# Performance work log

Measured on AMD Instinct MI355X. Metric: run time of the kernel, lower is better.

The kernel has to match this reference:

```python
import jax, jax.numpy as jnp
import numpy as np

D_MODEL = 4096
D_FF = 16384
BATCH = 1
SEQ = 1024


def setup_inputs() -> dict:
    key = jax.random.key(0)
    k_x, k_k, k_s = jax.random.split(key, 3)
    inputs = jax.random.normal(k_x, (BATCH, SEQ, D_MODEL), dtype=jnp.float32)
    # int4 quantized kernel, values in [-8, 8)
    kernel = jax.random.randint(k_k, (D_MODEL, D_FF), -8, 8, dtype=jnp.int32).astype(jnp.int4)
    # per-output-channel scale, shape (1, D_FF), strictly positive
    scale = jax.random.uniform(k_s, (1, D_FF), dtype=jnp.float32, minval=0.5, maxval=2.0)
    return {"inputs": inputs, "kernel": kernel, "scale": scale}


def reference(inputs, kernel, scale):
    # Dequantize: int4 kernel -> fp32, divide by per-channel scale
    kernel_f = kernel.astype(jnp.float32) / scale  # [D_MODEL, D_FF]
    # btd,df->btf
    return jnp.einsum("btd,df->btf", inputs, kernel_f)
```

## Files before the change

### kernel.cpp

```cpp
#include <hip/hip_runtime.h>
#include <hip/hip_bf16.h>

#define D_MODEL 4096
#define D_FF    16384
#define SEQ     1024

typedef __attribute__((ext_vector_type(4))) float          f32x4;
typedef __attribute__((ext_vector_type(4))) float          fvec4;
typedef __attribute__((ext_vector_type(8))) short          bf16x8;
typedef __attribute__((ext_vector_type(4))) unsigned short u16x4;

constexpr int BM = 256, BN = 256, BK = 64;
constexpr int NTHREADS = 512;
constexpr int NT = D_MODEL / BK;

__device__ __forceinline__ unsigned short f2bf(float f) {
    unsigned int u = __builtin_bit_cast(unsigned int, f);
    u += 0x7FFFu + ((u >> 16) & 1u);
    return (unsigned short)(u >> 16);
}

__device__ __forceinline__ float decode_kq(unsigned int w) {
    int iv = (int)w;
    return ((unsigned int)(iv + 8) <= 15u) ? (float)iv
                                           : __builtin_bit_cast(float, w);
}

__global__ __launch_bounds__(NTHREADS, 2)
void int4_gemm_kernel(const float* __restrict__ X, const unsigned int* __restrict__ Kq,
                      const float* __restrict__ scale, float* __restrict__ out)
{
    __shared__ short A_lds[2][BM * BK];
    __shared__ short B_lds[2][BN * BK];

    const int bid = blockIdx.x;
    const int bm  = (bid >> 3) & 3;
    const int bn  = (bid & 7) * 8 + (bid >> 5);

    const int tid  = threadIdx.x;
    const int lane = tid & 63;
    const int w    = tid >> 6;
    const int wr   = w >> 2;
    const int wc   = w & 3;
    const int lrow = lane & 15;
    const int lgrp = lane >> 4;

    const int row0 = bm * BM;
    const int col0 = bn * BN;

    const int a_m  = tid >> 4;
    const int a_f4 = tid & 15;
    const int b_n  = tid & 255;
    const int b_k8 = tid >> 8;

    f32x4 acc[8][4];
    #pragma unroll
    for (int i = 0; i < 8; ++i)
        #pragma unroll
        for (int j = 0; j < 4; ++j)
            acc[i][j] = (f32x4){0.f, 0.f, 0.f, 0.f};

    fvec4        aReg[8];
    unsigned int bReg[4][8];

    auto issue_loads = [&](int kt) {
        const int kbase = kt * BK;
        #pragma unroll
        for (int i = 0; i < 8; ++i) {
            int m = a_m + i * 32;
            aReg[i] = *reinterpret_cast<const fvec4*>(
                &X[(size_t)(row0 + m) * D_MODEL + kbase + a_f4 * 4]);
        }
        #pragma unroll
        for (int i = 0; i < 4; ++i) {
            int k8 = b_k8 + i * 2;
            const unsigned int* src =
                &Kq[(size_t)(kbase + k8 * 8) * D_FF + col0 + b_n];
            #pragma unroll
            for (int j = 0; j < 8; ++j) bReg[i][j] = src[(size_t)j * D_FF];
        }
    };

    auto write_lds = [&](int buf) {
        char* aB = (char*)A_lds[buf];
        char* bB = (char*)B_lds[buf];
        #pragma unroll
        for (int i = 0; i < 8; ++i) {
            int m = a_m + i * 32;
            u16x4 h;
            #pragma unroll
            for (int e = 0; e < 4; ++e) h[e] = f2bf(aReg[i][e]);
            int slot16 = a_f4 >> 1;
            int boff = m * 128 + ((slot16 ^ (m & 7)) * 16) + (a_f4 & 1) * 8;
            *reinterpret_cast<u16x4*>(aB + boff) = h;
        }
        #pragma unroll
        for (int i = 0; i < 4; ++i) {
            int k8 = b_k8 + i * 2;
            bf16x8 h;
            #pragma unroll
            for (int j = 0; j < 8; ++j) h[j] = (short)f2bf(decode_kq(bReg[i][j]));
            int boff = b_n * 128 + ((k8 ^ (b_n & 7)) * 16);
            *reinterpret_cast<bf16x8*>(bB + boff) = h;
        }
    };

    issue_loads(0);

    int cur = 0;
    for (int kt = 0; kt < NT; ++kt) {
        write_lds(cur);
        if (kt + 1 < NT) issue_loads(kt + 1);
        __syncthreads();

        const char* aB = (const char*)A_lds[cur];
        const char* bB = (const char*)B_lds[cur];
        #pragma unroll
        for (int ks = 0; ks < 2; ++ks) {
            bf16x8 afrag[8];
            bf16x8 bfrag[4];
            #pragma unroll
            for (int i = 0; i < 8; ++i) {
                int r = wr * 128 + i * 16 + lrow;
                int s = (ks * 4 + lgrp) ^ (r & 7);
                afrag[i] = *reinterpret_cast<const bf16x8*>(aB + r * 128 + s * 16);
            }
            #pragma unroll
            for (int j = 0; j < 4; ++j) {
                int n = wc * 64 + j * 16 + lrow;
                int s = (ks * 4 + lgrp) ^ (n & 7);
                bfrag[j] = *reinterpret_cast<const bf16x8*>(bB + n * 128 + s * 16);
            }
            #pragma unroll
            for (int i = 0; i < 8; ++i)
                #pragma unroll
                for (int j = 0; j < 4; ++j)
                    acc[i][j] = __builtin_amdgcn_mfma_f32_16x16x32_bf16(
                        afrag[i], bfrag[j], acc[i][j], 0, 0, 0);
        }
        cur ^= 1;
    }

    #pragma unroll
    for (int j = 0; j < 4; ++j) {
        int col = col0 + wc * 64 + j * 16 + lrow;
        float rs = 1.0f / scale[col];
        #pragma unroll
        for (int i = 0; i < 8; ++i) {
            int r0 = row0 + wr * 128 + i * 16 + lgrp * 4;
            #pragma unroll
            for (int r = 0; r < 4; ++r)
                out[(size_t)(r0 + r) * D_FF + col] = acc[i][j][r] * rs;
        }
    }
}

extern "C" void kernel_launch(void* const* d_in, const int* in_sizes, int n_in,
                              void* d_out, int out_size, void* d_ws, size_t ws_size,
                              hipStream_t stream) {
    const float*        X     = (const float*)d_in[0];
    const unsigned int* Kq    = (const unsigned int*)d_in[1];
    const float*        scale = (const float*)d_in[2];
    float*              out   = (float*)d_out;

    dim3 grid((SEQ / BM) * (D_FF / BN));
    dim3 block(NTHREADS);
    int4_gemm_kernel<<<grid, block, 0, stream>>>(X, Kq, scale, out);
}
```

Measured before the change: 521.5 us.

## Pre-convert activations to swizzled bf16 in workspace and restructure LDS pipeline

Adds a pre-pass kernel that converts the fp32 activations to bf16 once, already in the swizzled LDS tile layout, and stores them in the workspace. The GEMM then copies A tiles straight from the workspace into LDS, halving A global traffic and removing the per-tile conversions that each column block used to repeat. The main loop is reorganised so the LDS writes for the next tile are issued before the MFMAs on the current tile, with a hand-placed lgkmcnt wait and barrier. The int4 decode is simplified to truncate to bf16 instead of rounding. The cost is an extra kernel launch and a workspace requirement, with the old path kept as a fallback.

```diff
diff --git a/kernel.cpp b/kernel.cpp
--- a/kernel.cpp
+++ b/kernel.cpp
@@ -5,14 +5,16 @@
 #define D_FF    16384
 #define SEQ     1024
 
+typedef __attribute__((ext_vector_type(4))) float          fvec4;
 typedef __attribute__((ext_vector_type(4))) float          f32x4;
-typedef __attribute__((ext_vector_type(4))) float          fvec4;
+typedef __attribute__((ext_vector_type(4))) int            i32x4;
 typedef __attribute__((ext_vector_type(8))) short          bf16x8;
 typedef __attribute__((ext_vector_type(4))) unsigned short u16x4;
 
 constexpr int BM = 256, BN = 256, BK = 64;
 constexpr int NTHREADS = 512;
 constexpr int NT = D_MODEL / BK;
+constexpr size_t WS_A_BYTES = 4ull * NT * 32768;
 
 __device__ __forceinline__ unsigned short f2bf(float f) {
     unsigned int u = __builtin_bit_cast(unsigned int, f);
@@ -20,15 +22,41 @@
     return (unsigned short)(u >> 16);
 }
 
-__device__ __forceinline__ float decode_kq(unsigned int w) {
+__device__ __forceinline__ unsigned short kq_bf16(unsigned int w) {
     int iv = (int)w;
-    return ((unsigned int)(iv + 8) <= 15u) ? (float)iv
-                                           : __builtin_bit_cast(float, w);
-}
-
+    float fi = (float)iv;
+    unsigned int fw = ((unsigned int)(iv + 8) <= 15u)
+                        ? __builtin_bit_cast(unsigned int, fi) : w;
+    return (unsigned short)(fw >> 16);
+}
+
+__global__ __launch_bounds__(256)
+void preconv_A(const float* __restrict__ X, unsigned short* __restrict__ wsA)
+{
+    size_t u = (size_t)blockIdx.x * 256 + threadIdx.x;
+    size_t g = u * 8;
+    int bm    = (int)(g >> 21);
+    int r1    = (int)(g & 2097151);
+    int kt    = r1 >> 15;
+    int b     = r1 & 32767;
+    int m     = b >> 7;
+    int pslot = (b >> 4) & 7;
+    int t     = pslot ^ (m & 7);
+    int o     = (b >> 3) & 1;
+    int k     = t * 8 + o * 4;
+    const fvec4 v = *reinterpret_cast<const fvec4*>(
+        &X[(size_t)(bm * 256 + m) * D_MODEL + kt * BK + k]);
+    u16x4 h;
+    #pragma unroll
+    for (int e = 0; e < 4; ++e) h[e] = f2bf(v[e]);
+    *reinterpret_cast<u16x4*>((char*)wsA + g) = h;
+}
+
+template <bool PRE>
 __global__ __launch_bounds__(NTHREADS, 2)
 void int4_gemm_kernel(const float* __restrict__ X, const unsigned int* __restrict__ Kq,
-                      const float* __restrict__ scale, float* __restrict__ out)
+                      const float* __restrict__ scale, float* __restrict__ out,
+                      const unsigned short* __restrict__ wsA)
 {
     __shared__ short A_lds[2][BM * BK];
     __shared__ short B_lds[2][BN * BK];
@@ -48,8 +76,6 @@
     const int row0 = bm * BM;
     const int col0 = bn * BN;
 
-    const int a_m  = tid >> 4;
-    const int a_f4 = tid & 15;
     const int b_n  = tid & 255;
     const int b_k8 = tid >> 8;
 
@@ -60,61 +86,60 @@
         for (int j = 0; j < 4; ++j)
             acc[i][j] = (f32x4){0.f, 0.f, 0.f, 0.f};
 
-    fvec4        aReg[8];
     unsigned int bReg[4][8];
 
-    auto issue_loads = [&](int kt) {
+    auto issueB = [&](int kt) {
         const int kbase = kt * BK;
-        #pragma unroll
-        for (int i = 0; i < 8; ++i) {
-            int m = a_m + i * 32;
-            aReg[i] = *reinterpret_cast<const fvec4*>(
-                &X[(size_t)(row0 + m) * D_MODEL + kbase + a_f4 * 4]);
-        }
         #pragma unroll
         for (int i = 0; i < 4; ++i) {
             int k8 = b_k8 + i * 2;
-            const unsigned int* src =
-                &Kq[(size_t)(kbase + k8 * 8) * D_FF + col0 + b_n];
+            const unsigned int* src = &Kq[(size_t)(kbase + k8 * 8) * D_FF + col0 + b_n];
             #pragma unroll
             for (int j = 0; j < 8; ++j) bReg[i][j] = src[(size_t)j * D_FF];
         }
     };
-
-    auto write_lds = [&](int buf) {
-        char* aB = (char*)A_lds[buf];
-        char* bB = (char*)B_lds[buf];
-        #pragma unroll
-        for (int i = 0; i < 8; ++i) {
-            int m = a_m + i * 32;
-            u16x4 h;
-            #pragma unroll
-            for (int e = 0; e < 4; ++e) h[e] = f2bf(aReg[i][e]);
-            int slot16 = a_f4 >> 1;
-            int boff = m * 128 + ((slot16 ^ (m & 7)) * 16) + (a_f4 & 1) * 8;
-            *reinterpret_cast<u16x4*>(aB + boff) = h;
-        }
+    auto convertB = [&](short* Bbuf) {
+        char* bB = (char*)Bbuf;
         #pragma unroll
         for (int i = 0; i < 4; ++i) {
             int k8 = b_k8 + i * 2;
             bf16x8 h;
             #pragma unroll
-            for (int j = 0; j < 8; ++j) h[j] = (short)f2bf(decode_kq(bReg[i][j]));
+            for (int j = 0; j < 8; ++j) h[j] = (short)kq_bf16(bReg[i][j]);
             int boff = b_n * 128 + ((k8 ^ (b_n & 7)) * 16);
             *reinterpret_cast<bf16x8*>(bB + boff) = h;
         }
     };
-
-    issue_loads(0);
-
-    int cur = 0;
-    for (int kt = 0; kt < NT; ++kt) {
-        write_lds(cur);
-        if (kt + 1 < NT) issue_loads(kt + 1);
-        __syncthreads();
-
-        const char* aB = (const char*)A_lds[cur];
-        const char* bB = (const char*)B_lds[cur];
+    auto stageA = [&](int kt, short* Abuf) {
+        if constexpr (PRE) {
+            const char* src = (const char*)wsA + ((size_t)bm << 21) + ((size_t)kt << 15);
+            char* dst = (char*)Abuf;
+            #pragma unroll
+            for (int i = 0; i < 4; ++i) {
+                int off = i * 8192 + tid * 16;
+                *reinterpret_cast<i32x4*>(dst + off) =
+                    *reinterpret_cast<const i32x4*>(src + off);
+            }
+        } else {
+            const int a_m = tid >> 4, a_f4 = tid & 15;
+            const int kbase = kt * BK;
+            char* aB = (char*)Abuf;
+            #pragma unroll
+            for (int i = 0; i < 8; ++i) {
+                int m = a_m + i * 32;
+                const fvec4 v = *reinterpret_cast<const fvec4*>(
+                    &X[(size_t)(row0 + m) * D_MODEL + kbase + a_f4 * 4]);
+                u16x4 h;
+                #pragma unroll
+                for (int e = 0; e < 4; ++e) h[e] = f2bf(v[e]);
+                int boff = m * 128 + (((a_f4 >> 1) ^ (m & 7)) * 16) + (a_f4 & 1) * 8;
+                *reinterpret_cast<u16x4*>(aB + boff) = h;
+            }
+        }
+    };
+    auto mfma_step = [&](const short* Abuf, const short* Bbuf) {
+        const char* aB = (const char*)Abuf;
+        const char* bB = (const char*)Bbuf;
         #pragma unroll
         for (int ks = 0; ks < 2; ++ks) {
             bf16x8 afrag[8];
@@ -138,7 +163,27 @@
                     acc[i][j] = __builtin_amdgcn_mfma_f32_16x16x32_bf16(
                         afrag[i], bfrag[j], acc[i][j], 0, 0, 0);
         }
-        cur ^= 1;
+    };
+    auto tile_barrier = [&]() {
+        asm volatile("s_waitcnt lgkmcnt(0)" ::: "memory");
+        __builtin_amdgcn_s_barrier();
+    };
+
+    issueB(0);
+    stageA(0, A_lds[0]);
+    convertB(B_lds[0]);
+    issueB(1);
+    tile_barrier();
+
+    for (int kt = 0; kt < NT; kt += 2) {
+        if (kt + 1 < NT) { convertB(B_lds[1]); stageA(kt + 1, A_lds[1]); }
+        if (kt + 2 < NT) issueB(kt + 2);
+        mfma_step(A_lds[0], B_lds[0]);
+        tile_barrier();
+        if (kt + 2 < NT) { convertB(B_lds[0]); stageA(kt + 2, A_lds[0]); }
+        if (kt + 3 < NT) issueB(kt + 3);
+        mfma_step(A_lds[1], B_lds[1]);
+        tile_barrier();
     }
 
     #pragma unroll
@@ -165,5 +210,12 @@
 
     dim3 grid((SEQ / BM) * (D_FF / BN));
     dim3 block(NTHREADS);
-    int4_gemm_kernel<<<grid, block, 0, stream>>>(X, Kq, scale, out);
-}
+
+    if (ws_size >= WS_A_BYTES) {
+        unsigned short* wsA = (unsigned short*)d_ws;
+        preconv_A<<<dim3((unsigned)(WS_A_BYTES / 8 / 256)), dim3(256), 0, stream>>>(X, wsA);
+        int4_gemm_kernel<true><<<grid, block, 0, stream>>>(X, Kq, scale, out, wsA);
+    } else {
+        int4_gemm_kernel<false><<<grid, block, 0, stream>>>(X, Kq, scale, out, nullptr);
+    }
+}
```

Result: faster. 463.4 us (-11.1%).
